# Kernel tuning notes

Measured on AMD Instinct MI355X. Metric: run time of the kernel, lower is better.

The kernel has to match this reference:

```python
import jax, jax.numpy as jnp
import numpy as np

C = 10.0  # init kwarg


def _per_sample(g, dx, dy, sx, sy):
    # g: [2, h, w]; dx, dy, sx, sy scalars
    h, w = g.shape[1], g.shape[2]
    dy1f = jnp.floor(dy)
    dx1f = jnp.floor(dx)
    dy1 = dy1f.astype(jnp.int32)
    dx1 = dx1f.astype(jnp.int32)
    fy = dy - dy1f  # dy - dy1_f
    fx = dx - dx1f  # dx - dx1_f
    w22 = fx * fy
    w21 = fx * (1.0 - fy)
    w12 = (1.0 - fx) * fy
    w11 = (1.0 - fx) * (1.0 - fy)

    # S(ro, co)[c, i, j] == g[c, i+ro, j+co]  (wrapped; wrap region is masked out)
    S = lambda ro, co: jnp.roll(g, (-ro, -co), axis=(1, 2))

    # dx > 0 branch: delta(i,j) = g[i,j] - bilinear(g at (i+dy, j+dx))
    d_pos = g - (w22 * S(dy1 + 1, dx1 + 1) + w21 * S(dy1, dx1 + 1)
                 + w12 * S(dy1 + 1, dx1) + w11 * S(dy1, dx1))

    # dx <= 0 branch (faithful to the original index pattern):
    #   fx-weighted terms anchor at g[i+dy2, j+1], (1-fx)-weighted at g[i+dy2, j];
    #   sampled terms at rows i (fy) / i+1 (1-fy), column j - dx1.
    a2 = S(dy1 + 1, 1)
    a1 = S(dy1 + 1, 0)
    s_top = S(0, -dx1)
    s_bot = S(1, -dx1)
    d_neg = (w22 * (a2 - s_top) + w21 * (a2 - s_bot)
             + w12 * (a1 - s_top) + w11 * (a1 - s_bot))

    pos = dx > 0
    delta = jnp.where(pos, d_pos, d_neg)  # [2, h, w]

    ii = jnp.arange(h, dtype=jnp.int32)[:, None]
    jj = jnp.arange(w, dtype=jnp.int32)[None, :]
    rows = h - dy1 - 1                      # valid rows in both branches
    cols = jnp.where(pos, w - dx1 - 1, w + dx1)
    mask = (ii < rows) & (jj < cols)        # [h, w]
    count = (rows * cols).astype(g.dtype)

    val = delta[0] * sy + delta[1] * sx
    return jnp.sum(jnp.where(mask, val * val, jnp.zeros((), g.dtype))) / count


def setup_inputs() -> dict:
    key = jax.random.key(0)
    k1, k2, k3 = jax.random.split(key, 3)
    B, h, w = 32, 512, 512
    grid = jax.random.normal(k1, (B, 2, h, w), jnp.float32)
    u = jax.random.uniform(k2, (B, 3), jnp.float32)
    sign = jnp.where(u[:, 0] < 0.5, -1.0, 1.0)
    gt_x = sign * (0.2 + 0.3 * u[:, 1])   # dx = -C*gt_x -> |dx| in (2,5), both signs
    gt_y = 0.05 + 0.5 * u[:, 2]           # dy = C*gt_y in (0.5, 5.5)
    gt_sym_axis = jnp.stack([gt_x, gt_y], axis=1)
    gd_sym_axis = jax.random.normal(k3, (B, 2), jnp.float32)
    return {"grid": grid, "gt_sym_axis": gt_sym_axis, "gd_sym_axis": gd_sym_axis}


def reference(grid, gt_sym_axis, gd_sym_axis):
    dxs = -C * gt_sym_axis[:, 0]
    dys = C * gt_sym_axis[:, 1]
    losses = jax.vmap(_per_sample)(grid, dxs, dys,
                                   gd_sym_axis[:, 0], gd_sym_axis[:, 1])
    return jnp.mean(losses)
```

## Files before the change

### kernel.cpp

```cpp
#include <hip/hip_runtime.h>


#define GH 512
#define GW 512
#define GB 32
#define CH (GH * GW)
#define RPB 16
#define BLOCK 256
#define NBLK_X (GH / RPB)
#define NPART (NBLK_X * GB)

struct F4U { float x, y, z, w; };

__device__ __forceinline__ void load9(const float* __restrict__ p, float* o) {
    const F4U a = *(const F4U*)p;
    const F4U b = *(const F4U*)(p + 4);
    o[0]=a.x; o[1]=a.y; o[2]=a.z; o[3]=a.w;
    o[4]=b.x; o[5]=b.y; o[6]=b.z; o[7]=b.w;
    o[8] = p[8];
}

__device__ __forceinline__ void load8(const float* __restrict__ p, float* o) {
    const F4U a = *(const F4U*)p;
    const F4U b = *(const F4U*)(p + 4);
    o[0]=a.x; o[1]=a.y; o[2]=a.z; o[3]=a.w;
    o[4]=b.x; o[5]=b.y; o[6]=b.z; o[7]=b.w;
}

__global__ __launch_bounds__(BLOCK) void bilinear_sym_loss_stage1(
    const float* __restrict__ grid,
    const float* __restrict__ gt,
    const float* __restrict__ gd,
    float* __restrict__ partials)
{
    const int b = blockIdx.y;

    const float dx = -10.0f * gt[b * 2 + 0];
    const float dy =  10.0f * gt[b * 2 + 1];
    const float sx = gd[b * 2 + 0];
    const float sy = gd[b * 2 + 1];

    const float dy1f = floorf(dy);
    const float dx1f = floorf(dx);
    const int dy1 = (int)dy1f;
    const int dx1 = (int)dx1f;
    const float fy = dy - dy1f;
    const float fx = dx - dx1f;

    const bool pos = dx > 0.0f;
    const int rows = GH - dy1 - 1;
    const int cols = pos ? (GW - dx1 - 1) : (GW + dx1);

    const float omfx = 1.0f - fx;
    const float omfy = 1.0f - fy;
    const float w22 = fx * fy;
    const float w21 = fx * omfy;
    const float w12 = omfx * fy;
    const float w11 = omfx * omfy;

    const float* __restrict__ g0 = grid + (size_t)b * 2u * CH;

    const int tid = threadIdx.x;
    const int cc = tid & 63;
    const int rg = tid >> 6;
    const int i0 = blockIdx.x * RPB + rg * 4;

    int j0 = cc << 3;
    int kmin = 0;
    if (j0 > cols - 8) { kmin = j0 - (cols - 8); j0 = cols - 8; }

    float acc = 0.0f;

    if (pos) {
        if (i0 < rows) {
            const float* pa0 = g0 + (i0 + dy1) * GW + dx1 + j0;
            const float* pc0 = g0 + i0 * GW + j0;
            float P0[9], P1[9];
            load9(pa0, P0);
            load9(pa0 + CH, P1);
            #pragma unroll
            for (int r = 0; r < 4; ++r) {
                const int i = i0 + r;
                if (i >= rows) break;
                float B0[9], B1[9], C0[8], C1[8];
                load9(pa0 + (r + 1) * GW, B0);
                load9(pa0 + (r + 1) * GW + CH, B1);
                load8(pc0 + r * GW, C0);
                load8(pc0 + r * GW + CH, C1);
                #pragma unroll
                for (int k = 0; k < 8; ++k) {
                    float t0 = w11 * P0[k];
                    t0 = fmaf(w21, P0[k + 1], t0);
                    t0 = fmaf(w12, B0[k], t0);
                    t0 = fmaf(w22, B0[k + 1], t0);
                    const float d0 = C0[k] - t0;
                    float t1 = w11 * P1[k];
                    t1 = fmaf(w21, P1[k + 1], t1);
                    t1 = fmaf(w12, B1[k], t1);
                    t1 = fmaf(w22, B1[k + 1], t1);
                    const float d1 = C1[k] - t1;
                    float v = fmaf(d0, sy, d1 * sx);
                    v = (k >= kmin) ? v : 0.0f;
                    acc = fmaf(v, v, acc);
                }
                #pragma unroll
                for (int k = 0; k < 9; ++k) { P0[k] = B0[k]; P1[k] = B1[k]; }
            }
        }
    } else {
        if (i0 < rows) {
            const int jo = -dx1;
            const float* pt0 = g0 + i0 * GW + jo + j0;
            const float* pa0 = g0 + (i0 + dy1 + 1) * GW + j0;
            float T0[8], T1[8];
            load8(pt0, T0);
            load8(pt0 + CH, T1);
            #pragma unroll
            for (int r = 0; r < 4; ++r) {
                const int i = i0 + r;
                if (i >= rows) break;
                float S0[8], S1[8], A0[9], A1[9];
                load8(pt0 + (r + 1) * GW, S0);
                load8(pt0 + (r + 1) * GW + CH, S1);
                load9(pa0 + r * GW, A0);
                load9(pa0 + r * GW + CH, A1);
                #pragma unroll
                for (int k = 0; k < 8; ++k) {
                    float d0 = fx * A0[k + 1];
                    d0 = fmaf(omfx, A0[k], d0);
                    d0 = fmaf(-fy, T0[k], d0);
                    d0 = fmaf(-omfy, S0[k], d0);
                    float d1 = fx * A1[k + 1];
                    d1 = fmaf(omfx, A1[k], d1);
                    d1 = fmaf(-fy, T1[k], d1);
                    d1 = fmaf(-omfy, S1[k], d1);
                    float v = fmaf(d0, sy, d1 * sx);
                    v = (k >= kmin) ? v : 0.0f;
                    acc = fmaf(v, v, acc);
                }
                #pragma unroll
                for (int k = 0; k < 8; ++k) { T0[k] = S0[k]; T1[k] = S1[k]; }
            }
        }
    }

    for (int off = 32; off > 0; off >>= 1)
        acc += __shfl_down(acc, off, 64);

    __shared__ float wave_sums[BLOCK / 64];
    const int lane = tid & 63;
    const int wid = tid >> 6;
    if (lane == 0) wave_sums[wid] = acc;
    __syncthreads();

    if (tid == 0) {
        const float s = wave_sums[0] + wave_sums[1] + wave_sums[2] + wave_sums[3];
        const float count = (float)rows * (float)cols;
        const float scale = 1.0f / (count * (float)GB);
        partials[b * NBLK_X + blockIdx.x] = s * scale;
    }
}

__global__ __launch_bounds__(BLOCK) void bilinear_sym_loss_stage2(
    const float* __restrict__ partials,
    float* __restrict__ out)
{
    const int tid = threadIdx.x;
    float acc = 0.0f;
    for (int i = tid; i < NPART; i += BLOCK)
        acc += partials[i];

    for (int off = 32; off > 0; off >>= 1)
        acc += __shfl_down(acc, off, 64);

    __shared__ float wave_sums[BLOCK / 64];
    const int lane = tid & 63;
    const int wid = tid >> 6;
    if (lane == 0) wave_sums[wid] = acc;
    __syncthreads();

    if (tid == 0)
        out[0] = wave_sums[0] + wave_sums[1] + wave_sums[2] + wave_sums[3];
}

extern "C" void kernel_launch(void* const* d_in, const int* in_sizes, int n_in,
                              void* d_out, int out_size, void* d_ws, size_t ws_size,
                              hipStream_t stream) {
    const float* grid = (const float*)d_in[0];
    const float* gt   = (const float*)d_in[1];
    const float* gd   = (const float*)d_in[2];
    float* out = (float*)d_out;
    float* partials = (float*)d_ws;

    dim3 grid1(NBLK_X, GB);
    bilinear_sym_loss_stage1<<<grid1, dim3(BLOCK), 0, stream>>>(grid, gt, gd, partials);
    bilinear_sym_loss_stage2<<<dim3(1), dim3(BLOCK), 0, stream>>>(partials, out);
}
```

Measured before the change: 98.73 us.

## Software-pipeline row loads and swizzle block order across XCDs

Remaps the flat block index so consecutive hardware blocks, which are distributed round-robin over the eight chiplets, cover contiguous logical rows of the same sample. The goal is better L2 reuse of overlapping rows. The row loop now prefetches the next row's loads before computing the current one. Out-of-range rows are clamped and masked instead of breaking out of the loop. This trades higher register pressure and some redundant edge loads for more memory-level parallelism.

```diff
diff --git a/kernel.cpp b/kernel.cpp
--- a/kernel.cpp
+++ b/kernel.cpp
@@ -33,7 +33,10 @@
     const float* __restrict__ gd,
     float* __restrict__ partials)
 {
-    const int b = blockIdx.y;
+    const int flat = blockIdx.y * NBLK_X + blockIdx.x;
+    const int logi = (flat & 7) * (NPART >> 3) + (flat >> 3);
+    const int b  = logi >> 5;
+    const int bx = logi & (NBLK_X - 1);
 
     const float dx = -10.0f * gt[b * 2 + 0];
     const float dy =  10.0f * gt[b * 2 + 1];
@@ -63,7 +66,8 @@
     const int tid = threadIdx.x;
     const int cc = tid & 63;
     const int rg = tid >> 6;
-    const int i0 = blockIdx.x * RPB + rg * 4;
+    const int i0 = bx * RPB + rg * 4;
+    const int rc = rows - 1;
 
     int j0 = cc << 3;
     int kmin = 0;
@@ -72,74 +76,108 @@
     float acc = 0.0f;
 
     if (pos) {
-        if (i0 < rows) {
-            const float* pa0 = g0 + (i0 + dy1) * GW + dx1 + j0;
-            const float* pc0 = g0 + i0 * GW + j0;
-            float P0[9], P1[9];
-            load9(pa0, P0);
-            load9(pa0 + CH, P1);
-            #pragma unroll
-            for (int r = 0; r < 4; ++r) {
-                const int i = i0 + r;
-                if (i >= rows) break;
-                float B0[9], B1[9], C0[8], C1[8];
-                load9(pa0 + (r + 1) * GW, B0);
-                load9(pa0 + (r + 1) * GW + CH, B1);
-                load8(pc0 + r * GW, C0);
-                load8(pc0 + r * GW + CH, C1);
-                #pragma unroll
-                for (int k = 0; k < 8; ++k) {
-                    float t0 = w11 * P0[k];
-                    t0 = fmaf(w21, P0[k + 1], t0);
-                    t0 = fmaf(w12, B0[k], t0);
-                    t0 = fmaf(w22, B0[k + 1], t0);
-                    const float d0 = C0[k] - t0;
-                    float t1 = w11 * P1[k];
-                    t1 = fmaf(w21, P1[k + 1], t1);
-                    t1 = fmaf(w12, B1[k], t1);
-                    t1 = fmaf(w22, B1[k + 1], t1);
-                    const float d1 = C1[k] - t1;
-                    float v = fmaf(d0, sy, d1 * sx);
-                    v = (k >= kmin) ? v : 0.0f;
-                    acc = fmaf(v, v, acc);
-                }
-                #pragma unroll
-                for (int k = 0; k < 9; ++k) { P0[k] = B0[k]; P1[k] = B1[k]; }
+        const float* baseA = g0 + dx1 + j0;
+        const float* baseC = g0 + j0;
+        float P0[9], P1[9];
+        {
+            const int ip = min(i0, rc) + dy1;
+            load9(baseA + ip * GW, P0);
+            load9(baseA + ip * GW + CH, P1);
+        }
+        float B0[9], B1[9], C0[8], C1[8];
+        {
+            const int ic = min(i0, rc);
+            load9(baseA + (ic + dy1 + 1) * GW, B0);
+            load9(baseA + (ic + dy1 + 1) * GW + CH, B1);
+            load8(baseC + ic * GW, C0);
+            load8(baseC + ic * GW + CH, C1);
+        }
+        #pragma unroll
+        for (int r = 0; r < 4; ++r) {
+            float N0[9], N1[9], D0[8], D1[8];
+            if (r < 3) {
+                const int ic = min(i0 + r + 1, rc);
+                load9(baseA + (ic + dy1 + 1) * GW, N0);
+                load9(baseA + (ic + dy1 + 1) * GW + CH, N1);
+                load8(baseC + ic * GW, D0);
+                load8(baseC + ic * GW + CH, D1);
+            }
+            const bool rowok = (i0 + r) < rows;
+            #pragma unroll
+            for (int k = 0; k < 8; ++k) {
+                float t0 = w11 * P0[k];
+                t0 = fmaf(w21, P0[k + 1], t0);
+                t0 = fmaf(w12, B0[k], t0);
+                t0 = fmaf(w22, B0[k + 1], t0);
+                const float d0 = C0[k] - t0;
+                float t1 = w11 * P1[k];
+                t1 = fmaf(w21, P1[k + 1], t1);
+                t1 = fmaf(w12, B1[k], t1);
+                t1 = fmaf(w22, B1[k + 1], t1);
+                const float d1 = C1[k] - t1;
+                float v = fmaf(d0, sy, d1 * sx);
+                v = (rowok && k >= kmin) ? v : 0.0f;
+                acc = fmaf(v, v, acc);
+            }
+            #pragma unroll
+            for (int k = 0; k < 9; ++k) { P0[k] = B0[k]; P1[k] = B1[k]; }
+            if (r < 3) {
+                #pragma unroll
+                for (int k = 0; k < 9; ++k) { B0[k] = N0[k]; B1[k] = N1[k]; }
+                #pragma unroll
+                for (int k = 0; k < 8; ++k) { C0[k] = D0[k]; C1[k] = D1[k]; }
             }
         }
     } else {
-        if (i0 < rows) {
-            const int jo = -dx1;
-            const float* pt0 = g0 + i0 * GW + jo + j0;
-            const float* pa0 = g0 + (i0 + dy1 + 1) * GW + j0;
-            float T0[8], T1[8];
-            load8(pt0, T0);
-            load8(pt0 + CH, T1);
-            #pragma unroll
-            for (int r = 0; r < 4; ++r) {
-                const int i = i0 + r;
-                if (i >= rows) break;
-                float S0[8], S1[8], A0[9], A1[9];
-                load8(pt0 + (r + 1) * GW, S0);
-                load8(pt0 + (r + 1) * GW + CH, S1);
-                load9(pa0 + r * GW, A0);
-                load9(pa0 + r * GW + CH, A1);
-                #pragma unroll
-                for (int k = 0; k < 8; ++k) {
-                    float d0 = fx * A0[k + 1];
-                    d0 = fmaf(omfx, A0[k], d0);
-                    d0 = fmaf(-fy, T0[k], d0);
-                    d0 = fmaf(-omfy, S0[k], d0);
-                    float d1 = fx * A1[k + 1];
-                    d1 = fmaf(omfx, A1[k], d1);
-                    d1 = fmaf(-fy, T1[k], d1);
-                    d1 = fmaf(-omfy, S1[k], d1);
-                    float v = fmaf(d0, sy, d1 * sx);
-                    v = (k >= kmin) ? v : 0.0f;
-                    acc = fmaf(v, v, acc);
-                }
-                #pragma unroll
-                for (int k = 0; k < 8; ++k) { T0[k] = S0[k]; T1[k] = S1[k]; }
+        const int jo = -dx1;
+        const float* baseT = g0 + jo + j0;
+        const float* baseA = g0 + j0;
+        float T0[8], T1[8];
+        {
+            const int it = min(i0, rc);
+            load8(baseT + it * GW, T0);
+            load8(baseT + it * GW + CH, T1);
+        }
+        float S0[8], S1[8], A0[9], A1[9];
+        {
+            const int ic = min(i0, rc);
+            load8(baseT + (ic + 1) * GW, S0);
+            load8(baseT + (ic + 1) * GW + CH, S1);
+            load9(baseA + (ic + dy1 + 1) * GW, A0);
+            load9(baseA + (ic + dy1 + 1) * GW + CH, A1);
+        }
+        #pragma unroll
+        for (int r = 0; r < 4; ++r) {
+            float NS0[8], NS1[8], NA0[9], NA1[9];
+            if (r < 3) {
+                const int ic = min(i0 + r + 1, rc);
+                load8(baseT + (ic + 1) * GW, NS0);
+                load8(baseT + (ic + 1) * GW + CH, NS1);
+                load9(baseA + (ic + dy1 + 1) * GW, NA0);
+                load9(baseA + (ic + dy1 + 1) * GW + CH, NA1);
+            }
+            const bool rowok = (i0 + r) < rows;
+            #pragma unroll
+            for (int k = 0; k < 8; ++k) {
+                float d0 = fx * A0[k + 1];
+                d0 = fmaf(omfx, A0[k], d0);
+                d0 = fmaf(-fy, T0[k], d0);
+                d0 = fmaf(-omfy, S0[k], d0);
+                float d1 = fx * A1[k + 1];
+                d1 = fmaf(omfx, A1[k], d1);
+                d1 = fmaf(-fy, T1[k], d1);
+                d1 = fmaf(-omfy, S1[k], d1);
+                float v = fmaf(d0, sy, d1 * sx);
+                v = (rowok && k >= kmin) ? v : 0.0f;
+                acc = fmaf(v, v, acc);
+            }
+            #pragma unroll
+            for (int k = 0; k < 8; ++k) { T0[k] = S0[k]; T1[k] = S1[k]; }
+            if (r < 3) {
+                #pragma unroll
+                for (int k = 0; k < 8; ++k) { S0[k] = NS0[k]; S1[k] = NS1[k]; }
+                #pragma unroll
+                for (int k = 0; k < 9; ++k) { A0[k] = NA0[k]; A1[k] = NA1[k]; }
             }
         }
     }
@@ -157,7 +195,7 @@
         const float s = wave_sums[0] + wave_sums[1] + wave_sums[2] + wave_sums[3];
         const float count = (float)rows * (float)cols;
         const float scale = 1.0f / (count * (float)GB);
-        partials[b * NBLK_X + blockIdx.x] = s * scale;
+        partials[b * NBLK_X + bx] = s * scale;
     }
 }
 
```

New measurement: 98.02 us. Within noise of the previous version (-0.7%).
